# Kernel optimization log

Measured on AMD Instinct MI355X. Metric: run time of the kernel, lower is better.

The kernel has to match this reference:

```python
import jax, jax.numpy as jnp
import numpy as np

N = 2048       # agent nodes
D = 128        # latent_dim
H = 64         # hidden width of edge MLP


def setup_inputs() -> dict:
    key = jax.random.key(0)
    k_z, k_w1, k_w2, k_eps = jax.random.split(key, 4)
    z = jax.random.normal(k_z, (N + 1, D), dtype=jnp.float32)
    # nn.Linear(3D, 64) weight stored as (in, out) for right-multiplication
    W1 = jax.random.normal(k_w1, (3 * D, H), dtype=jnp.float32) / np.sqrt(3 * D)
    b1 = jnp.zeros((H,), dtype=jnp.float32)
    W2 = jax.random.normal(k_w2, (H, 1), dtype=jnp.float32) / np.sqrt(H)
    b2 = jnp.zeros((1,), dtype=jnp.float32)
    # uniform noise standing in for torch.rand_like(w) in the training branch
    eps = jax.random.uniform(k_eps, (N, N), dtype=jnp.float32)
    return {"z": z, "W1": W1, "b1": b1, "W2": W2, "b2": b2, "eps": eps}


def reference(z, W1, b1, W2, b2, eps):
    # z: (N+1, D); last row is the task node
    agent = z[:-1]                      # (N, D)
    task = z[-1]                        # (D,)
    # Decompose Linear(3D->H) over the concat [h_i, h_j, task]:
    # combined @ W1 = h_i @ W1a + h_j @ W1b + task @ W1c
    W1a, W1b, W1c = W1[:D], W1[D:2 * D], W1[2 * D:]
    pi = agent @ W1a                    # (N, H) row term
    pj = agent @ W1b                    # (N, H) col term
    pt = task @ W1c + b1                # (H,)   shared task term + bias
    h = jax.nn.relu(pi[:, None, :] + pj[None, :, :] + pt)   # (N, N, H)
    w = jnp.einsum('ijh,h->ij', h, W2[:, 0]) + b2[0]         # (N, N) edge logits
    # Gumbel-sigmoid (training branch), temperature = 1.0
    e = eps + 1e-8
    gumbel = jnp.log(e) - jnp.log(1.0 - e)
    return jax.nn.sigmoid(w + gumbel)
```

## Files before the change

kernel.cpp:

```cpp
#include <hip/hip_runtime.h>

#define NN 2048
#define DD 128
#define HH 64

__global__ __launch_bounds__(256) void proj_kernel(
    const float* __restrict__ z, const float* __restrict__ W1,
    const float* __restrict__ b1, float* __restrict__ pi, float* __restrict__ pjt)
{
    __shared__ float sA[16][DD];
    __shared__ float sT[DD];
    const int t = threadIdx.x;
    const int rowBase = blockIdx.x * 16;

    #pragma unroll
    for (int c = 0; c < 2; ++c) {
        int idx = c * 256 + t;
        int rr  = idx >> 5;
        int kq  = idx & 31;
        float4 v = *(const float4*)(z + (rowBase + rr) * DD + kq * 4);
        *(float4*)(&sA[rr][kq * 4]) = v;
    }
    if (t < DD / 4) {
        float4 v = *(const float4*)(z + (size_t)NN * DD + t * 4);
        *(float4*)(&sT[t * 4]) = v;
    }
    __syncthreads();

    const int h  = t & 63;
    const int rg = t >> 6;

    float ai[4] = {0.f, 0.f, 0.f, 0.f};
    float aj[4] = {0.f, 0.f, 0.f, 0.f};
    float at = 0.f;
    #pragma unroll 4
    for (int k = 0; k < DD; ++k) {
        const float w1a = W1[k * HH + h];
        const float w1b = W1[(DD + k) * HH + h];
        const float w1c = W1[(2 * DD + k) * HH + h];
        at = fmaf(sT[k], w1c, at);
        #pragma unroll
        for (int a = 0; a < 4; ++a) {
            const float av = sA[rg * 4 + a][k];
            ai[a] = fmaf(av, w1a, ai[a]);
            aj[a] = fmaf(av, w1b, aj[a]);
        }
    }
    const float ptv = at + b1[h];
    #pragma unroll
    for (int a = 0; a < 4; ++a) {
        const int row = rowBase + rg * 4 + a;
        pi[row * HH + h]  = ai[a];
        pjt[row * HH + h] = aj[a] + ptv;
    }
}

__global__ __launch_bounds__(256) void pair_kernel(
    const float* __restrict__ pi, const float* __restrict__ pjt,
    const float* __restrict__ W2, const float* __restrict__ b2,
    const float* __restrict__ eps, float* __restrict__ out)
{
    __shared__ float sPi[HH][68];
    __shared__ float sPj[HH][68];
    __shared__ float sW2[HH];

    const int t  = threadIdx.x;
    const int i0 = blockIdx.y * 64;
    const int j0 = blockIdx.x * 64;

    #pragma unroll
    for (int c = 0; c < 4; ++c) {
        int idx = c * 256 + t;
        int ii  = idx >> 4;
        int hq  = idx & 15;
        float4 v = *(const float4*)(pi  + (size_t)(i0 + ii) * HH + hq * 4);
        sPi[hq * 4 + 0][ii] = v.x;
        sPi[hq * 4 + 1][ii] = v.y;
        sPi[hq * 4 + 2][ii] = v.z;
        sPi[hq * 4 + 3][ii] = v.w;
        float4 u = *(const float4*)(pjt + (size_t)(j0 + ii) * HH + hq * 4);
        sPj[hq * 4 + 0][ii] = u.x;
        sPj[hq * 4 + 1][ii] = u.y;
        sPj[hq * 4 + 2][ii] = u.z;
        sPj[hq * 4 + 3][ii] = u.w;
    }
    if (t < HH) sW2[t] = W2[t];
    __syncthreads();

    const int lane = t & 63;
    const int wv   = t >> 6;
    const int iloc = (wv & 1) * 32 + (lane & 7) * 4;
    const int jloc = (wv >> 1) * 32 + (lane >> 3) * 4;

    float acc[4][4];
    #pragma unroll
    for (int a = 0; a < 4; ++a)
        #pragma unroll
        for (int b = 0; b < 4; ++b) acc[a][b] = 0.f;

    #pragma unroll 8
    for (int h = 0; h < HH; ++h) {
        const float4 av = *(const float4*)(&sPi[h][iloc]);
        const float4 bv = *(const float4*)(&sPj[h][jloc]);
        const float w2h = sW2[h];
        const float a4[4] = {av.x, av.y, av.z, av.w};
        const float b4[4] = {bv.x, bv.y, bv.z, bv.w};
        #pragma unroll
        for (int a = 0; a < 4; ++a)
            #pragma unroll
            for (int b = 0; b < 4; ++b)
                acc[a][b] = fmaf(fmaxf(a4[a] + b4[b], 0.f), w2h, acc[a][b]);
    }

    const float b2v = b2[0];
    #pragma unroll
    for (int a = 0; a < 4; ++a) {
        const int gi = i0 + iloc + a;
        const size_t base = (size_t)gi * NN + j0 + jloc;
        const float4 e4 = *(const float4*)(eps + base);
        float4 o;
        {
            float e = e4.x + 1e-8f, w = acc[a][0] + b2v;
            float ex = __expf(-w);
            o.x = __fdividef(e, e + (1.f - e) * ex);
        }
        {
            float e = e4.y + 1e-8f, w = acc[a][1] + b2v;
            float ex = __expf(-w);
            o.y = __fdividef(e, e + (1.f - e) * ex);
        }
        {
            float e = e4.z + 1e-8f, w = acc[a][2] + b2v;
            float ex = __expf(-w);
            o.z = __fdividef(e, e + (1.f - e) * ex);
        }
        {
            float e = e4.w + 1e-8f, w = acc[a][3] + b2v;
            float ex = __expf(-w);
            o.w = __fdividef(e, e + (1.f - e) * ex);
        }
        *(float4*)(out + base) = o;
    }
}

extern "C" void kernel_launch(void* const* d_in, const int* in_sizes, int n_in,
                              void* d_out, int out_size, void* d_ws, size_t ws_size,
                              hipStream_t stream) {
    const float* z   = (const float*)d_in[0];
    const float* W1  = (const float*)d_in[1];
    const float* b1  = (const float*)d_in[2];
    const float* W2  = (const float*)d_in[3];
    const float* b2  = (const float*)d_in[4];
    const float* eps = (const float*)d_in[5];
    float* out = (float*)d_out;

    float* pi  = (float*)d_ws;
    float* pjt = pi + (size_t)NN * HH;

    proj_kernel<<<NN / 16, 256, 0, stream>>>(z, W1, b1, pi, pjt);
    pair_kernel<<<dim3(NN / 64, NN / 64), 256, 0, stream>>>(pi, pjt, W2, b2, eps, out);
}
```

Measured before the change: 115.4 us.

## Enlarge pair tile to 128x64, prefetch eps before compute, vectorize transposes

The pair kernel tile grows to 128 rows by 64 columns, so each thread computes an 8x4 output block instead of 4x4. This raises the ratio of FMAs to LDS reads. The eps loads are issued before the h loop so their global latency overlaps the shared-memory setup and compute. The LDS transpose stores now use float4, and W2 is read straight from global/scalar memory instead of shared. The larger register tile, with launch_bounds(256,2), risks register pressure and halves the number of blocks.

```diff
diff --git a/kernel.cpp b/kernel.cpp
--- a/kernel.cpp
+++ b/kernel.cpp
@@ -55,89 +55,101 @@
     }
 }
 
-__global__ __launch_bounds__(256) void pair_kernel(
+__global__ __launch_bounds__(256, 2) void pair_kernel(
     const float* __restrict__ pi, const float* __restrict__ pjt,
     const float* __restrict__ W2, const float* __restrict__ b2,
     const float* __restrict__ eps, float* __restrict__ out)
 {
-    __shared__ float sPi[HH][68];
+    __shared__ float sPi[HH][132];
     __shared__ float sPj[HH][68];
-    __shared__ float sW2[HH];
 
     const int t  = threadIdx.x;
-    const int i0 = blockIdx.y * 64;
+    const int i0 = blockIdx.y * 128;
     const int j0 = blockIdx.x * 64;
 
     #pragma unroll
-    for (int c = 0; c < 4; ++c) {
-        int idx = c * 256 + t;
-        int ii  = idx >> 4;
-        int hq  = idx & 15;
-        float4 v = *(const float4*)(pi  + (size_t)(i0 + ii) * HH + hq * 4);
-        sPi[hq * 4 + 0][ii] = v.x;
-        sPi[hq * 4 + 1][ii] = v.y;
-        sPi[hq * 4 + 2][ii] = v.z;
-        sPi[hq * 4 + 3][ii] = v.w;
-        float4 u = *(const float4*)(pjt + (size_t)(j0 + ii) * HH + hq * 4);
-        sPj[hq * 4 + 0][ii] = u.x;
-        sPj[hq * 4 + 1][ii] = u.y;
-        sPj[hq * 4 + 2][ii] = u.z;
-        sPj[hq * 4 + 3][ii] = u.w;
+    for (int c = 0; c < 2; ++c) {
+        const int g  = c * 256 + t;
+        const int hq = g & 15;
+        const int ig = g >> 4;
+        const float* src = pi + (size_t)(i0 + ig * 4) * HH + hq * 4;
+        float4 v0 = *(const float4*)(src);
+        float4 v1 = *(const float4*)(src + HH);
+        float4 v2 = *(const float4*)(src + 2 * HH);
+        float4 v3 = *(const float4*)(src + 3 * HH);
+        *(float4*)(&sPi[hq * 4 + 0][ig * 4]) = make_float4(v0.x, v1.x, v2.x, v3.x);
+        *(float4*)(&sPi[hq * 4 + 1][ig * 4]) = make_float4(v0.y, v1.y, v2.y, v3.y);
+        *(float4*)(&sPi[hq * 4 + 2][ig * 4]) = make_float4(v0.z, v1.z, v2.z, v3.z);
+        *(float4*)(&sPi[hq * 4 + 3][ig * 4]) = make_float4(v0.w, v1.w, v2.w, v3.w);
     }
-    if (t < HH) sW2[t] = W2[t];
-    __syncthreads();
+    {
+        const int hq = t & 15;
+        const int jg = t >> 4;
+        const float* src = pjt + (size_t)(j0 + jg * 4) * HH + hq * 4;
+        float4 v0 = *(const float4*)(src);
+        float4 v1 = *(const float4*)(src + HH);
+        float4 v2 = *(const float4*)(src + 2 * HH);
+        float4 v3 = *(const float4*)(src + 3 * HH);
+        *(float4*)(&sPj[hq * 4 + 0][jg * 4]) = make_float4(v0.x, v1.x, v2.x, v3.x);
+        *(float4*)(&sPj[hq * 4 + 1][jg * 4]) = make_float4(v0.y, v1.y, v2.y, v3.y);
+        *(float4*)(&sPj[hq * 4 + 2][jg * 4]) = make_float4(v0.z, v1.z, v2.z, v3.z);
+        *(float4*)(&sPj[hq * 4 + 3][jg * 4]) = make_float4(v0.w, v1.w, v2.w, v3.w);
+    }
 
     const int lane = t & 63;
     const int wv   = t >> 6;
-    const int iloc = (wv & 1) * 32 + (lane & 7) * 4;
-    const int jloc = (wv >> 1) * 32 + (lane >> 3) * 4;
+    const int ib   = (wv >> 1) * 64 + (lane >> 3) * 8;
+    const int jb   = (wv & 1) * 32 + (lane & 7) * 4;
 
-    float acc[4][4];
+    float4 eps4[8];
     #pragma unroll
-    for (int a = 0; a < 4; ++a)
+    for (int r = 0; r < 8; ++r)
+        eps4[r] = *(const float4*)(eps + (size_t)(i0 + ib + r) * NN + (j0 + jb));
+
+    __syncthreads();
+
+    float acc[8][4];
+    #pragma unroll
+    for (int r = 0; r < 8; ++r)
         #pragma unroll
-        for (int b = 0; b < 4; ++b) acc[a][b] = 0.f;
+        for (int c = 0; c < 4; ++c) acc[r][c] = 0.f;
 
-    #pragma unroll 8
+    #pragma unroll 4
     for (int h = 0; h < HH; ++h) {
-        const float4 av = *(const float4*)(&sPi[h][iloc]);
-        const float4 bv = *(const float4*)(&sPj[h][jloc]);
-        const float w2h = sW2[h];
-        const float a4[4] = {av.x, av.y, av.z, av.w};
-        const float b4[4] = {bv.x, bv.y, bv.z, bv.w};
+        const float4 a0 = *(const float4*)(&sPi[h][ib]);
+        const float4 a1 = *(const float4*)(&sPi[h][ib + 4]);
+        const float4 bv = *(const float4*)(&sPj[h][jb]);
+        const float w2h = W2[h];
+        const float ai[8] = {a0.x, a0.y, a0.z, a0.w, a1.x, a1.y, a1.z, a1.w};
+        const float bj[4] = {bv.x, bv.y, bv.z, bv.w};
         #pragma unroll
-        for (int a = 0; a < 4; ++a)
+        for (int r = 0; r < 8; ++r)
             #pragma unroll
-            for (int b = 0; b < 4; ++b)
-                acc[a][b] = fmaf(fmaxf(a4[a] + b4[b], 0.f), w2h, acc[a][b]);
+            for (int c = 0; c < 4; ++c)
+                acc[r][c] = fmaf(fmaxf(ai[r] + bj[c], 0.f), w2h, acc[r][c]);
     }
 
     const float b2v = b2[0];
     #pragma unroll
-    for (int a = 0; a < 4; ++a) {
-        const int gi = i0 + iloc + a;
-        const size_t base = (size_t)gi * NN + j0 + jloc;
-        const float4 e4 = *(const float4*)(eps + base);
+    for (int r = 0; r < 8; ++r) {
+        const size_t base = (size_t)(i0 + ib + r) * NN + (j0 + jb);
+        const float4 e4 = eps4[r];
         float4 o;
         {
-            float e = e4.x + 1e-8f, w = acc[a][0] + b2v;
-            float ex = __expf(-w);
-            o.x = __fdividef(e, e + (1.f - e) * ex);
+            float e = e4.x + 1e-8f, w = acc[r][0] + b2v;
+            o.x = __fdividef(e, e + (1.f - e) * __expf(-w));
         }
         {
-            float e = e4.y + 1e-8f, w = acc[a][1] + b2v;
-            float ex = __expf(-w);
-            o.y = __fdividef(e, e + (1.f - e) * ex);
+            float e = e4.y + 1e-8f, w = acc[r][1] + b2v;
+            o.y = __fdividef(e, e + (1.f - e) * __expf(-w));
         }
         {
-            float e = e4.z + 1e-8f, w = acc[a][2] + b2v;
-            float ex = __expf(-w);
-            o.z = __fdividef(e, e + (1.f - e) * ex);
+            float e = e4.z + 1e-8f, w = acc[r][2] + b2v;
+            o.z = __fdividef(e, e + (1.f - e) * __expf(-w));
         }
         {
-            float e = e4.w + 1e-8f, w = acc[a][3] + b2v;
-            float ex = __expf(-w);
-            o.w = __fdividef(e, e + (1.f - e) * ex);
+            float e = e4.w + 1e-8f, w = acc[r][3] + b2v;
+            o.w = __fdividef(e, e + (1.f - e) * __expf(-w));
         }
         *(float4*)(out + base) = o;
     }
@@ -158,5 +170,5 @@
     float* pjt = pi + (size_t)NN * HH;
 
     proj_kernel<<<NN / 16, 256, 0, stream>>>(z, W1, b1, pi, pjt);
-    pair_kernel<<<dim3(NN / 64, NN / 64), 256, 0, stream>>>(pi, pjt, W2, b2, eps, out);
+    pair_kernel<<<dim3(NN / 64, NN / 128), 256, 0, stream>>>(pi, pjt, W2, b2, eps, out);
 }
```

After: 115.5 us. No clear change (+0.1%).
